# Kernel tuning notes

Hardware: AMD Instinct MI355X
Metric: run time of the kernel (lower is better)

The kernel has to match this reference:

```python
import jax, jax.numpy as jnp
import numpy as np

N_NODES = 100000
N_EDGES = 1600000
IN_FEATS = 128
HIDDEN = 32
HEADS = 4
OUT_FEATS = 64
NEG_SLOPE = 0.2  # DGL GATConv default negative_slope


def gat_layer(x, src, dst, fc_w, attn_l, attn_r, bias, n_nodes):
    """DGL GATConv: fc -> per-node attn terms -> edge leaky_relu -> segment softmax -> scatter-sum.
    x: [N, F_in]; fc_w: [F_in, H*D]; attn_l/attn_r: [H, D]; bias: [H*D].
    Returns [N, H, D]."""
    H, D = attn_l.shape
    feat = (x @ fc_w).reshape(-1, H, D)            # [N, H, D]
    el = jnp.sum(feat * attn_l, axis=-1)           # [N, H]
    er = jnp.sum(feat * attn_r, axis=-1)           # [N, H]
    e = jax.nn.leaky_relu(el[src] + er[dst], NEG_SLOPE)   # [E, H]
    # segment softmax over incoming edges of each dst node
    m = jax.ops.segment_max(e, dst, num_segments=n_nodes)  # [N, H] (-inf for 0-in-degree)
    ex = jnp.exp(e - m[dst])                       # [E, H]
    denom = jax.ops.segment_sum(ex, dst, num_segments=n_nodes)  # [N, H]
    alpha = ex / denom[dst]                        # [E, H]
    msg = feat[src] * alpha[:, :, None]            # [E, H, D]
    out = jax.ops.segment_sum(msg, dst, num_segments=n_nodes)   # [N, H, D]
    return out + bias.reshape(1, H, D)


def setup_inputs() -> dict:
    key = jax.random.key(0)
    ks = jax.random.split(key, 12)
    features = jax.random.normal(ks[0], (N_NODES, IN_FEATS), dtype=jnp.float32)
    src = jax.random.randint(ks[1], (N_EDGES,), 0, N_NODES)
    dst = jax.random.randint(ks[2], (N_EDGES,), 0, N_NODES)
    s1 = 1.0 / np.sqrt(IN_FEATS)
    s2 = 1.0 / np.sqrt(HIDDEN * HEADS)
    fc1_w = jax.random.normal(ks[3], (IN_FEATS, HIDDEN * HEADS), dtype=jnp.float32) * s1
    attn_l1 = jax.random.normal(ks[4], (HEADS, HIDDEN), dtype=jnp.float32) * s1
    attn_r1 = jax.random.normal(ks[5], (HEADS, HIDDEN), dtype=jnp.float32) * s1
    bias1 = jnp.zeros((HIDDEN * HEADS,), dtype=jnp.float32)
    fc2_w = jax.random.normal(ks[6], (HIDDEN * HEADS, OUT_FEATS), dtype=jnp.float32) * s2
    attn_l2 = jax.random.normal(ks[7], (1, OUT_FEATS), dtype=jnp.float32) * s2
    attn_r2 = jax.random.normal(ks[8], (1, OUT_FEATS), dtype=jnp.float32) * s2
    bias2 = jnp.zeros((OUT_FEATS,), dtype=jnp.float32)
    return {"features": features, "src": src, "dst": dst,
            "fc1_w": fc1_w, "attn_l1": attn_l1, "attn_r1": attn_r1, "bias1": bias1,
            "fc2_w": fc2_w, "attn_l2": attn_l2, "attn_r2": attn_r2, "bias2": bias2}


def reference(features, src, dst, fc1_w, attn_l1, attn_r1, bias1, fc2_w, attn_l2, attn_r2, bias2):
    n = features.shape[0]
    x = gat_layer(features, src, dst, fc1_w, attn_l1, attn_r1, bias1, n)  # [N, H, D1]
    x = jax.nn.elu(x.reshape(n, -1))                                     # [N, H*D1]
    x = gat_layer(x, src, dst, fc2_w, attn_l2, attn_r2, bias2, n)        # [N, 1, D2]
    return x.mean(axis=1)                                                # [N, D2]
```

## Files before the change

### kernel.cpp

```cpp
#include <hip/hip_runtime.h>
#include <math.h>

typedef __attribute__((ext_vector_type(8))) short bf16x8;
typedef __attribute__((ext_vector_type(4))) float f32x4;

#define MAXDEG 64
#define NPART 8


__device__ __forceinline__ unsigned int packbf2(float a, float b) {
    unsigned int ua = __float_as_uint(a);
    ua = (ua + 0x7FFFu + ((ua >> 16) & 1u)) >> 16;
    unsigned int ub = __float_as_uint(b);
    ub = (ub + 0x7FFFu + ((ub >> 16) & 1u)) & 0xFFFF0000u;
    return ua | ub;
}

__device__ __forceinline__ unsigned short bf16r(float x) {
    unsigned int u = __float_as_uint(x);
    u = (u + 0x7FFFu + ((u >> 16) & 1u)) >> 16;
    return (unsigned short)u;
}

__device__ __forceinline__ void bf2_fma(unsigned int u, float w, float& a0, float& a1) {
    a0 += w * __uint_as_float(u << 16);
    a1 += w * __uint_as_float(u & 0xFFFF0000u);
}


__global__ __launch_bounds__(256) void k_gemm1_rank(const int* __restrict__ dst,
                                                    int* __restrict__ cnt8,
                                                    int* __restrict__ rank, int e,
                                                    const float* __restrict__ X,
                                                    const float* __restrict__ W,
                                                    const float* __restrict__ attn_l,
                                                    const float* __restrict__ attn_r,
                                                    unsigned short* __restrict__ feat,
                                                    float* __restrict__ el,
                                                    float* __restrict__ er, int n) {
    __shared__ unsigned short sX[64 * 128];
    __shared__ unsigned short sWT[128 * 128];
    int t = threadIdx.x;
    int ebase = blockIdx.x * 1024 + t;
    int* cpart = cnt8 + (size_t)(blockIdx.x & (NPART - 1)) * n;
    int d0 = (ebase < e) ? dst[ebase] : -1;
    int d1 = (ebase + 256 < e) ? dst[ebase + 256] : -1;
    int d2 = (ebase + 512 < e) ? dst[ebase + 512] : -1;
    int d3 = (ebase + 768 < e) ? dst[ebase + 768] : -1;

    int node0 = blockIdx.x * 64;
    {
        const float4* Xv = (const float4*)X;
        char* sXb = (char*)sX;
        for (int i = t; i < 2048; i += 256) {
            int r = i >> 5, q = i & 31;
            int node = node0 + r;
            float4 val = make_float4(0.f, 0.f, 0.f, 0.f);
            if (node < n) val = Xv[(size_t)node * 32 + q];
            unsigned off = (unsigned)(r * 256 + q * 8) ^ (unsigned)((r & 7) << 4);
            *(uint2*)(sXb + off) = make_uint2(packbf2(val.x, val.y), packbf2(val.z, val.w));
        }
    }
    {
        char* sWb = (char*)sWT;
        int c = t & 127;
        int kp0 = (t >> 7) * 32;
        for (int j = 0; j < 32; ++j) {
            int kp = kp0 + j;
            float f0 = W[(2 * kp) * 128 + c];
            float f1 = W[(2 * kp + 1) * 128 + c];
            unsigned off = (unsigned)(c * 256 + kp * 4) ^ (unsigned)((c & 7) << 4);
            *(unsigned*)(sWb + off) = packbf2(f0, f1);
        }
    }
    __syncthreads();
    int p0 = 0, p1 = 0, p2 = 0, p3 = 0;
    if (d0 >= 0) p0 = atomicAdd(&cpart[d0], 1);
    if (d1 >= 0) p1 = atomicAdd(&cpart[d1], 1);
    if (d2 >= 0) p2 = atomicAdd(&cpart[d2], 1);
    if (d3 >= 0) p3 = atomicAdd(&cpart[d3], 1);

    int w = t >> 6;
    int l = t & 63;
    int lr = l & 15;
    int lk = l >> 4;
    f32x4 acc[8] = {};
    {
        const char* sXb = (const char*)sX;
        const char* sWb = (const char*)sWT;
        int arow = w * 16 + lr;
        unsigned aswz = (unsigned)((arow & 7) << 4);
        unsigned abase = (unsigned)(arow * 256 + lk * 16);
#pragma unroll
        for (int kb = 0; kb < 4; ++kb) {
            bf16x8 afrag = *(const bf16x8*)(sXb + ((abase + kb * 64) ^ aswz));
#pragma unroll
            for (int cb = 0; cb < 8; ++cb) {
                int col = cb * 16 + lr;
                unsigned boff = (unsigned)(col * 256 + kb * 64 + lk * 16) ^ (unsigned)((col & 7) << 4);
                bf16x8 bfrag = *(const bf16x8*)(sWb + boff);
                acc[cb] = __builtin_amdgcn_mfma_f32_16x16x32_bf16(afrag, bfrag, acc[cb], 0, 0, 0);
            }
        }
    }
    {
        float alv[8], arv[8];
#pragma unroll
        for (int cb = 0; cb < 8; ++cb) {
            alv[cb] = attn_l[cb * 16 + lr];
            arv[cb] = attn_r[cb * 16 + lr];
        }
#pragma unroll
        for (int r = 0; r < 4; ++r) {
            int node = node0 + w * 16 + lk * 4 + r;
            float pl[4], pr[4];
#pragma unroll
            for (int h = 0; h < 4; ++h) {
                pl[h] = acc[2 * h][r] * alv[2 * h] + acc[2 * h + 1][r] * alv[2 * h + 1];
                pr[h] = acc[2 * h][r] * arv[2 * h] + acc[2 * h + 1][r] * arv[2 * h + 1];
            }
#pragma unroll
            for (int off = 1; off < 16; off <<= 1) {
#pragma unroll
                for (int h = 0; h < 4; ++h) {
                    pl[h] += __shfl_xor(pl[h], off);
                    pr[h] += __shfl_xor(pr[h], off);
                }
            }
            if (node < n && lr < 4) {
                el[node * 4 + lr] = pl[lr];
                er[node * 4 + lr] = pr[lr];
            }
        }
    }
    if (d0 >= 0) rank[ebase] = p0;
    if (d1 >= 0) rank[ebase + 256] = p1;
    if (d2 >= 0) rank[ebase + 512] = p2;
    if (d3 >= 0) rank[ebase + 768] = p3;

    __syncthreads();
    unsigned short* sOut = sWT;
#pragma unroll
    for (int cb = 0; cb < 8; ++cb)
#pragma unroll
        for (int r = 0; r < 4; ++r)
            sOut[(w * 16 + lk * 4 + r) * 128 + cb * 16 + lr] = bf16r(acc[cb][r]);
    __syncthreads();
    for (int i = t; i < 1024; i += 256) {
        int r = i >> 4, q = i & 15;
        int node = node0 + r;
        if (node < n)
            *(uint4*)(feat + (size_t)node * 128 + q * 8) = *(const uint4*)(sOut + r * 128 + q * 8);
    }
}


__global__ __launch_bounds__(256) void k_merge(const int* __restrict__ cnt8,
                                               int* __restrict__ base8,
                                               int* __restrict__ cnt, int n) {
    int i = blockIdx.x * 256 + threadIdx.x;
    if (i >= n) return;
    int s = 0;
    int b[NPART];
#pragma unroll
    for (int p = 0; p < NPART; ++p) {
        b[p] = s;
        s += cnt8[(size_t)p * n + i];
    }
    cnt[i] = s;
#pragma unroll
    for (int p = 0; p < NPART; ++p) base8[i * NPART + p] = b[p];
}


__global__ __launch_bounds__(256) void k_place(const int* __restrict__ src,
                                               const int* __restrict__ dst,
                                               const int* __restrict__ rank,
                                               const int* __restrict__ base8,
                                               int* __restrict__ csrF, int e) {
    int base = blockIdx.x * 1024 + threadIdx.x;
#pragma unroll
    for (int j = 0; j < 4; ++j) {
        int i = base + j * 256;
        if (i < e) {
            int part = (i >> 10) & (NPART - 1);
            int d = dst[i];
            int slot = base8[d * NPART + part] + rank[i];
            if (slot < MAXDEG) csrF[(size_t)d * MAXDEG + slot] = src[i];
        }
    }
}


__global__ __launch_bounds__(256) void k_gemm2(const unsigned short* __restrict__ X2,
                                               const float* __restrict__ W,
                                               const float* __restrict__ attn_l,
                                               const float* __restrict__ attn_r,
                                               unsigned short* __restrict__ feat,
                                               float* __restrict__ el,
                                               float* __restrict__ er, int n) {
    __shared__ unsigned short sX[64 * 128];
    __shared__ unsigned short sWT[64 * 128];
    int t = threadIdx.x;
    int node0 = blockIdx.x * 64;
    {
        const uint2* Xv = (const uint2*)X2;
        char* sXb = (char*)sX;
        for (int i = t; i < 2048; i += 256) {
            int r = i >> 5, q = i & 31;
            int node = node0 + r;
            uint2 val = make_uint2(0u, 0u);
            if (node < n) val = Xv[(size_t)node * 32 + q];
            unsigned off = (unsigned)(r * 256 + q * 8) ^ (unsigned)((r & 7) << 4);
            *(uint2*)(sXb + off) = val;
        }
    }
    {
        char* sWb = (char*)sWT;
        int c = t & 63;
        int kp0 = (t >> 6) * 16;
#pragma unroll
        for (int j = 0; j < 16; ++j) {
            int kp = kp0 + j;
            float f0 = W[(2 * kp) * 64 + c];
            float f1 = W[(2 * kp + 1) * 64 + c];
            unsigned off = (unsigned)(c * 256 + kp * 4) ^ (unsigned)((c & 7) << 4);
            *(unsigned*)(sWb + off) = packbf2(f0, f1);
        }
    }
    __syncthreads();

    int w = t >> 6;
    int l = t & 63;
    int lr = l & 15;
    int lk = l >> 4;
    f32x4 acc[4] = {};
    {
        const char* sXb = (const char*)sX;
        const char* sWb = (const char*)sWT;
        int arow = w * 16 + lr;
        unsigned aswz = (unsigned)((arow & 7) << 4);
        unsigned abase = (unsigned)(arow * 256 + lk * 16);
#pragma unroll
        for (int kb = 0; kb < 4; ++kb) {
            bf16x8 afrag = *(const bf16x8*)(sXb + ((abase + kb * 64) ^ aswz));
#pragma unroll
            for (int cb = 0; cb < 4; ++cb) {
                int col = cb * 16 + lr;
                unsigned boff = (unsigned)(col * 256 + kb * 64 + lk * 16) ^ (unsigned)((col & 7) << 4);
                bf16x8 bfrag = *(const bf16x8*)(sWb + boff);
                acc[cb] = __builtin_amdgcn_mfma_f32_16x16x32_bf16(afrag, bfrag, acc[cb], 0, 0, 0);
            }
        }
    }
    {
        float alv[4], arv[4];
#pragma unroll
        for (int cb = 0; cb < 4; ++cb) {
            alv[cb] = attn_l[cb * 16 + lr];
            arv[cb] = attn_r[cb * 16 + lr];
        }
#pragma unroll
        for (int r = 0; r < 4; ++r) {
            int node = node0 + w * 16 + lk * 4 + r;
            float pl = 0.f, pr = 0.f;
#pragma unroll
            for (int cb = 0; cb < 4; ++cb) {
                pl += acc[cb][r] * alv[cb];
                pr += acc[cb][r] * arv[cb];
            }
#pragma unroll
            for (int off = 1; off < 16; off <<= 1) {
                pl += __shfl_xor(pl, off);
                pr += __shfl_xor(pr, off);
            }
            if (node < n && lr == 0) {
                el[node] = pl;
                er[node] = pr;
            }
        }
    }
    __syncthreads();
    unsigned short* sOut = sWT;
#pragma unroll
    for (int cb = 0; cb < 4; ++cb)
#pragma unroll
        for (int r = 0; r < 4; ++r)
            sOut[(w * 16 + lk * 4 + r) * 64 + cb * 16 + lr] = bf16r(acc[cb][r]);
    __syncthreads();
    for (int i = t; i < 512; i += 256) {
        int r = i >> 3, q = i & 7;
        int node = node0 + r;
        if (node < n)
            *(uint4*)(feat + (size_t)node * 64 + q * 8) = *(const uint4*)(sOut + r * 64 + q * 8);
    }
}


__global__ __launch_bounds__(256) void k_gather1(const int* __restrict__ cnt,
                                                 const int* __restrict__ csrF,
                                                 const unsigned short* __restrict__ feat,
                                                 const float* __restrict__ el,
                                                 const float* __restrict__ er,
                                                 const float* __restrict__ bias,
                                                 unsigned short* __restrict__ xout, int n) {
    int wid = (blockIdx.x * blockDim.x + threadIdx.x) >> 6;
    int lane = threadIdx.x & 63;
    if (wid >= n) return;
    int g = lane >> 4;
    int dl = lane & 15;
    int h = dl >> 2;
    int deg = cnt[wid];
    if (deg > MAXDEG) deg = MAXDEG;
    int start = wid * MAXDEG, end = start + deg;
    float erh = er[wid * 4 + h];
    float A[8] = {};
    float D = 0.f;
    int slot = start + g;
    for (; slot + 12 < end; slot += 16) {
        int s0 = csrF[slot];
        int s1 = csrF[slot + 4];
        int s2 = csrF[slot + 8];
        int s3 = csrF[slot + 12];
        float e0 = el[s0 * 4 + h];
        float e1 = el[s1 * 4 + h];
        float e2 = el[s2 * 4 + h];
        float e3 = el[s3 * 4 + h];
        uint4 f0 = *(const uint4*)(feat + (size_t)s0 * 128 + 8 * dl);
        uint4 f1 = *(const uint4*)(feat + (size_t)s1 * 128 + 8 * dl);
        uint4 f2 = *(const uint4*)(feat + (size_t)s2 * 128 + 8 * dl);
        uint4 f3 = *(const uint4*)(feat + (size_t)s3 * 128 + 8 * dl);
        e0 += erh; e0 = (e0 > 0.f) ? e0 : 0.2f * e0; float w0 = __expf(e0);
        e1 += erh; e1 = (e1 > 0.f) ? e1 : 0.2f * e1; float w1 = __expf(e1);
        e2 += erh; e2 = (e2 > 0.f) ? e2 : 0.2f * e2; float w2 = __expf(e2);
        e3 += erh; e3 = (e3 > 0.f) ? e3 : 0.2f * e3; float w3 = __expf(e3);
        D += w0 + w1 + w2 + w3;
        bf2_fma(f0.x, w0, A[0], A[1]); bf2_fma(f0.y, w0, A[2], A[3]);
        bf2_fma(f0.z, w0, A[4], A[5]); bf2_fma(f0.w, w0, A[6], A[7]);
        bf2_fma(f1.x, w1, A[0], A[1]); bf2_fma(f1.y, w1, A[2], A[3]);
        bf2_fma(f1.z, w1, A[4], A[5]); bf2_fma(f1.w, w1, A[6], A[7]);
        bf2_fma(f2.x, w2, A[0], A[1]); bf2_fma(f2.y, w2, A[2], A[3]);
        bf2_fma(f2.z, w2, A[4], A[5]); bf2_fma(f2.w, w2, A[6], A[7]);
        bf2_fma(f3.x, w3, A[0], A[1]); bf2_fma(f3.y, w3, A[2], A[3]);
        bf2_fma(f3.z, w3, A[4], A[5]); bf2_fma(f3.w, w3, A[6], A[7]);
    }
    for (; slot < end; slot += 4) {
        int s = csrF[slot];
        float e0 = el[s * 4 + h];
        uint4 f = *(const uint4*)(feat + (size_t)s * 128 + 8 * dl);
        e0 += erh; e0 = (e0 > 0.f) ? e0 : 0.2f * e0; float w = __expf(e0);
        D += w;
        bf2_fma(f.x, w, A[0], A[1]); bf2_fma(f.y, w, A[2], A[3]);
        bf2_fma(f.z, w, A[4], A[5]); bf2_fma(f.w, w, A[6], A[7]);
    }
#pragma unroll
    for (int off = 16; off < 64; off <<= 1) {
#pragma unroll
        for (int j = 0; j < 8; ++j) A[j] += __shfl_xor(A[j], off);
        D += __shfl_xor(D, off);
    }
    if (g == 0) {
        float rd = (D > 0.f) ? 1.f / D : 0.f;
        const float* bp = bias + 8 * dl;
        float4 b0 = *(const float4*)bp;
        float4 b1 = *(const float4*)(bp + 4);
        float o[8];
        o[0] = A[0] * rd + b0.x; o[1] = A[1] * rd + b0.y;
        o[2] = A[2] * rd + b0.z; o[3] = A[3] * rd + b0.w;
        o[4] = A[4] * rd + b1.x; o[5] = A[5] * rd + b1.y;
        o[6] = A[6] * rd + b1.z; o[7] = A[7] * rd + b1.w;
#pragma unroll
        for (int j = 0; j < 8; ++j) o[j] = (o[j] > 0.f) ? o[j] : (__expf(o[j]) - 1.f);
        uint4 pk;
        pk.x = packbf2(o[0], o[1]);
        pk.y = packbf2(o[2], o[3]);
        pk.z = packbf2(o[4], o[5]);
        pk.w = packbf2(o[6], o[7]);
        *(uint4*)(xout + (size_t)wid * 128 + 8 * dl) = pk;
    }
}


__global__ __launch_bounds__(256) void k_gather2(const int* __restrict__ cnt,
                                                 const int* __restrict__ csrF,
                                                 const unsigned short* __restrict__ feat,
                                                 const float* __restrict__ el,
                                                 const float* __restrict__ er,
                                                 const float* __restrict__ bias,
                                                 float* __restrict__ out, int n) {
    int wid = (blockIdx.x * blockDim.x + threadIdx.x) >> 6;
    int lane = threadIdx.x & 63;
    if (wid >= n) return;
    int g = lane >> 3;
    int dl = lane & 7;
    int deg = cnt[wid];
    if (deg > MAXDEG) deg = MAXDEG;
    int start = wid * MAXDEG, end = start + deg;
    float erv = er[wid];
    float A[8] = {};
    float D = 0.f;
    int slot = start + g;
    for (; slot + 8 < end; slot += 16) {
        int s0 = csrF[slot];
        int s1 = csrF[slot + 8];
        float e0 = el[s0];
        float e1 = el[s1];
        uint4 f0 = *(const uint4*)(feat + (size_t)s0 * 64 + 8 * dl);
        uint4 f1 = *(const uint4*)(feat + (size_t)s1 * 64 + 8 * dl);
        e0 += erv; e0 = (e0 > 0.f) ? e0 : 0.2f * e0; float w0 = __expf(e0);
        e1 += erv; e1 = (e1 > 0.f) ? e1 : 0.2f * e1; float w1 = __expf(e1);
        D += w0 + w1;
        bf2_fma(f0.x, w0, A[0], A[1]); bf2_fma(f0.y, w0, A[2], A[3]);
        bf2_fma(f0.z, w0, A[4], A[5]); bf2_fma(f0.w, w0, A[6], A[7]);
        bf2_fma(f1.x, w1, A[0], A[1]); bf2_fma(f1.y, w1, A[2], A[3]);
        bf2_fma(f1.z, w1, A[4], A[5]); bf2_fma(f1.w, w1, A[6], A[7]);
    }
    if (slot < end) {
        int s = csrF[slot];
        float e0 = el[s];
        uint4 f = *(const uint4*)(feat + (size_t)s * 64 + 8 * dl);
        e0 += erv; e0 = (e0 > 0.f) ? e0 : 0.2f * e0; float w = __expf(e0);
        D += w;
        bf2_fma(f.x, w, A[0], A[1]); bf2_fma(f.y, w, A[2], A[3]);
        bf2_fma(f.z, w, A[4], A[5]); bf2_fma(f.w, w, A[6], A[7]);
    }
#pragma unroll
    for (int off = 8; off < 64; off <<= 1) {
#pragma unroll
        for (int j = 0; j < 8; ++j) A[j] += __shfl_xor(A[j], off);
        D += __shfl_xor(D, off);
    }
    if (g == 0) {
        float rd = (D > 0.f) ? 1.f / D : 0.f;
        const float* bp = bias + 8 * dl;
        float4 b0 = *(const float4*)bp;
        float4 b1 = *(const float4*)(bp + 4);
        float4 o0, o1;
        o0.x = A[0] * rd + b0.x; o0.y = A[1] * rd + b0.y;
        o0.z = A[2] * rd + b0.z; o0.w = A[3] * rd + b0.w;
        o1.x = A[4] * rd + b1.x; o1.y = A[5] * rd + b1.y;
        o1.z = A[6] * rd + b1.z; o1.w = A[7] * rd + b1.w;
        float* op = out + (size_t)wid * 64 + 8 * dl;
        *(float4*)op = o0;
        *(float4*)(op + 4) = o1;
    }
}


extern "C" void kernel_launch(void* const* d_in, const int* in_sizes, int n_in,
                              void* d_out, int out_size, void* d_ws, size_t ws_size,
                              hipStream_t stream) {
    const float* features = (const float*)d_in[0];
    const int* src = (const int*)d_in[1];
    const int* dst = (const int*)d_in[2];
    const float* fc1_w = (const float*)d_in[3];
    const float* attn_l1 = (const float*)d_in[4];
    const float* attn_r1 = (const float*)d_in[5];
    const float* bias1 = (const float*)d_in[6];
    const float* fc2_w = (const float*)d_in[7];
    const float* attn_l2 = (const float*)d_in[8];
    const float* attn_r2 = (const float*)d_in[9];
    const float* bias2 = (const float*)d_in[10];
    const int N = in_sizes[0] / 128;
    const int E = in_sizes[1];

    char* ws = (char*)d_ws;
    size_t off = 0;
    auto alloc = [&](size_t bytes) {
        void* p = ws + off;
        off = (off + bytes + 255) & ~(size_t)255;
        return p;
    };
    int* cnt8 = (int*)alloc((size_t)N * NPART * 4);
    int* base8 = (int*)alloc((size_t)N * NPART * 4);
    int* cnt = (int*)alloc((size_t)N * 4);
    int* rank = (int*)alloc((size_t)E * 4);
    int* csrF = (int*)alloc((size_t)N * MAXDEG * 4);
    unsigned short* x2 = (unsigned short*)alloc((size_t)N * 128 * 2);
    size_t l1_off = off;
    unsigned short* feat1 = (unsigned short*)alloc((size_t)N * 128 * 2);
    float* el1 = (float*)alloc((size_t)N * 4 * 4);
    float* er1 = (float*)alloc((size_t)N * 4 * 4);
    off = l1_off;
    unsigned short* feat2 = (unsigned short*)alloc((size_t)N * 64 * 2);
    float* el2 = (float*)alloc((size_t)N * 4);
    float* er2 = (float*)alloc((size_t)N * 4);

    hipMemsetAsync(cnt8, 0, (size_t)N * NPART * 4, stream);

    int ngemm = (N + 63) / 64;
    int nedge = (E + 1023) / 1024;
    int nblk = (ngemm > nedge) ? ngemm : nedge;
    k_gemm1_rank<<<nblk, 256, 0, stream>>>(dst, cnt8, rank, E,
                                           features, fc1_w, attn_l1, attn_r1,
                                           feat1, el1, er1, N);
    k_merge<<<(N + 255) / 256, 256, 0, stream>>>(cnt8, base8, cnt, N);
    k_place<<<(E + 1023) / 1024, 256, 0, stream>>>(src, dst, rank, base8, csrF, E);

    int nwave = (N + 3) / 4;
    k_gather1<<<nwave, 256, 0, stream>>>(cnt, csrF, feat1, el1, er1, bias1, x2, N);
    k_gemm2<<<(N + 63) / 64, 256, 0, stream>>>(x2, fc2_w, attn_l2, attn_r2, feat2, el2, er2, N);
    k_gather2<<<nwave, 256, 0, stream>>>(cnt, csrF, feat2, el2, er2, bias2, (float*)d_out, N);
}
```

Baseline: 258.2 us.

## Replace partitioned count/merge CSR build with single atomic-fill placement

The edge-bucketing scheme is simplified: instead of per-partition atomic counts inside the GEMM kernel, a merge kernel, and a rank-based placement, k_place now claims slots directly with one atomicAdd per edge on a single fill counter and writes the source index. This removes the merge kernel, the rank and base8 arrays and their memory traffic, and decouples the GEMM from the edge work. In exchange, all atomics go to one counter array, which raises contention, and the order of neighbours within each row becomes nondeterministic, so floating-point sums may vary between runs.

```diff
diff --git a/kernel.cpp b/kernel.cpp
--- a/kernel.cpp
+++ b/kernel.cpp
@@ -5,7 +5,6 @@
 typedef __attribute__((ext_vector_type(4))) float f32x4;
 
 #define MAXDEG 64
-#define NPART 8
 
 
 __device__ __forceinline__ unsigned int packbf2(float a, float b) {
@@ -28,26 +27,16 @@
 }
 
 
-__global__ __launch_bounds__(256) void k_gemm1_rank(const int* __restrict__ dst,
-                                                    int* __restrict__ cnt8,
-                                                    int* __restrict__ rank, int e,
-                                                    const float* __restrict__ X,
-                                                    const float* __restrict__ W,
-                                                    const float* __restrict__ attn_l,
-                                                    const float* __restrict__ attn_r,
-                                                    unsigned short* __restrict__ feat,
-                                                    float* __restrict__ el,
-                                                    float* __restrict__ er, int n) {
+__global__ __launch_bounds__(256) void k_gemm1(const float* __restrict__ X,
+                                               const float* __restrict__ W,
+                                               const float* __restrict__ attn_l,
+                                               const float* __restrict__ attn_r,
+                                               unsigned short* __restrict__ feat,
+                                               float* __restrict__ el,
+                                               float* __restrict__ er, int n) {
     __shared__ unsigned short sX[64 * 128];
     __shared__ unsigned short sWT[128 * 128];
     int t = threadIdx.x;
-    int ebase = blockIdx.x * 1024 + t;
-    int* cpart = cnt8 + (size_t)(blockIdx.x & (NPART - 1)) * n;
-    int d0 = (ebase < e) ? dst[ebase] : -1;
-    int d1 = (ebase + 256 < e) ? dst[ebase + 256] : -1;
-    int d2 = (ebase + 512 < e) ? dst[ebase + 512] : -1;
-    int d3 = (ebase + 768 < e) ? dst[ebase + 768] : -1;
-
     int node0 = blockIdx.x * 64;
     {
         const float4* Xv = (const float4*)X;
@@ -74,11 +63,6 @@
         }
     }
     __syncthreads();
-    int p0 = 0, p1 = 0, p2 = 0, p3 = 0;
-    if (d0 >= 0) p0 = atomicAdd(&cpart[d0], 1);
-    if (d1 >= 0) p1 = atomicAdd(&cpart[d1], 1);
-    if (d2 >= 0) p2 = atomicAdd(&cpart[d2], 1);
-    if (d3 >= 0) p3 = atomicAdd(&cpart[d3], 1);
 
     int w = t >> 6;
     int l = t & 63;
@@ -133,11 +117,6 @@
             }
         }
     }
-    if (d0 >= 0) rank[ebase] = p0;
-    if (d1 >= 0) rank[ebase + 256] = p1;
-    if (d2 >= 0) rank[ebase + 512] = p2;
-    if (d3 >= 0) rank[ebase + 768] = p3;
-
     __syncthreads();
     unsigned short* sOut = sWT;
 #pragma unroll
@@ -155,40 +134,24 @@
 }
 
 
-__global__ __launch_bounds__(256) void k_merge(const int* __restrict__ cnt8,
-                                               int* __restrict__ base8,
-                                               int* __restrict__ cnt, int n) {
-    int i = blockIdx.x * 256 + threadIdx.x;
-    if (i >= n) return;
-    int s = 0;
-    int b[NPART];
-#pragma unroll
-    for (int p = 0; p < NPART; ++p) {
-        b[p] = s;
-        s += cnt8[(size_t)p * n + i];
-    }
-    cnt[i] = s;
-#pragma unroll
-    for (int p = 0; p < NPART; ++p) base8[i * NPART + p] = b[p];
-}
-
-
 __global__ __launch_bounds__(256) void k_place(const int* __restrict__ src,
                                                const int* __restrict__ dst,
-                                               const int* __restrict__ rank,
-                                               const int* __restrict__ base8,
+                                               int* __restrict__ fill,
                                                int* __restrict__ csrF, int e) {
     int base = blockIdx.x * 1024 + threadIdx.x;
+    int d[4], s[4], p[4];
 #pragma unroll
     for (int j = 0; j < 4; ++j) {
         int i = base + j * 256;
-        if (i < e) {
-            int part = (i >> 10) & (NPART - 1);
-            int d = dst[i];
-            int slot = base8[d * NPART + part] + rank[i];
-            if (slot < MAXDEG) csrF[(size_t)d * MAXDEG + slot] = src[i];
-        }
-    }
+        d[j] = (i < e) ? dst[i] : -1;
+        s[j] = (i < e) ? src[i] : 0;
+    }
+#pragma unroll
+    for (int j = 0; j < 4; ++j)
+        if (d[j] >= 0) p[j] = atomicAdd(&fill[d[j]], 1);
+#pragma unroll
+    for (int j = 0; j < 4; ++j)
+        if (d[j] >= 0 && p[j] < MAXDEG) csrF[(size_t)d[j] * MAXDEG + p[j]] = s[j];
 }
 
 
@@ -471,10 +434,7 @@
         off = (off + bytes + 255) & ~(size_t)255;
         return p;
     };
-    int* cnt8 = (int*)alloc((size_t)N * NPART * 4);
-    int* base8 = (int*)alloc((size_t)N * NPART * 4);
-    int* cnt = (int*)alloc((size_t)N * 4);
-    int* rank = (int*)alloc((size_t)E * 4);
+    int* fill = (int*)alloc((size_t)N * 4);
     int* csrF = (int*)alloc((size_t)N * MAXDEG * 4);
     unsigned short* x2 = (unsigned short*)alloc((size_t)N * 128 * 2);
     size_t l1_off = off;
@@ -486,19 +446,14 @@
     float* el2 = (float*)alloc((size_t)N * 4);
     float* er2 = (float*)alloc((size_t)N * 4);
 
-    hipMemsetAsync(cnt8, 0, (size_t)N * NPART * 4, stream);
-
-    int ngemm = (N + 63) / 64;
-    int nedge = (E + 1023) / 1024;
-    int nblk = (ngemm > nedge) ? ngemm : nedge;
-    k_gemm1_rank<<<nblk, 256, 0, stream>>>(dst, cnt8, rank, E,
-                                           features, fc1_w, attn_l1, attn_r1,
-                                           feat1, el1, er1, N);
-    k_merge<<<(N + 255) / 256, 256, 0, stream>>>(cnt8, base8, cnt, N);
-    k_place<<<(E + 1023) / 1024, 256, 0, stream>>>(src, dst, rank, base8, csrF, E);
+    hipMemsetAsync(fill, 0, (size_t)N * 4, stream);
+
+    k_gemm1<<<(N + 63) / 64, 256, 0, stream>>>(features, fc1_w, attn_l1, attn_r1,
+                                               feat1, el1, er1, N);
+    k_place<<<(E + 1023) / 1024, 256, 0, stream>>>(src, dst, fill, csrF, E);
 
     int nwave = (N + 3) / 4;
-    k_gather1<<<nwave, 256, 0, stream>>>(cnt, csrF, feat1, el1, er1, bias1, x2, N);
+    k_gather1<<<nwave, 256, 0, stream>>>(fill, csrF, feat1, el1, er1, bias1, x2, N);
     k_gemm2<<<(N + 63) / 64, 256, 0, stream>>>(x2, fc2_w, attn_l2, attn_r2, feat2, el2, er2, N);
-    k_gather2<<<nwave, 256, 0, stream>>>(cnt, csrF, feat2, el2, er2, bias2, (float*)d_out, N);
-}
+    k_gather2<<<nwave, 256, 0, stream>>>(fill, csrF, feat2, el2, er2, bias2, (float*)d_out, N);
+}
```

Measured after the change: 296.1 us. 1.15x slower.
